# Optimization experiments

Hardware: AMD Instinct MI355X
Metric: run time of the kernel (lower is better)

Reference implementation:

```python
import jax, jax.numpy as jnp
import numpy as np

F = 6      # num_factors (== nodes per sample)
H = 32     # hidden_dim
B = 65536  # batch of samples (vectorized version of the per-sample Python loop)


def setup_inputs() -> dict:
    key = jax.random.key(0)
    ks = jax.random.split(key, 20)
    p = lambda k, shape: (jax.random.normal(k, shape, dtype=jnp.float32) * 0.1)
    inp = {
        "factors": jax.random.normal(ks[0], (B, F, F), dtype=jnp.float32),
        # CausalStructureLearner.node_encoder: Linear(F, H)
        "Wn": p(ks[1], (F, H)), "bn": p(ks[2], (H,)),
        # edge_predictor: Linear(2H, H) -> ReLU -> Linear(H, 1) -> Sigmoid
        "We1": p(ks[3], (2 * H, H)), "be1": p(ks[4], (H,)),
        "We2": p(ks[5], (H, 1)), "be2": p(ks[6], (1,)),
        # DynamicsPredictor.dynamics_net: F->H->H->F
        "Wd1": p(ks[7], (F, H)), "bd1": p(ks[8], (H,)),
        "Wd2": p(ks[9], (H, H)), "bd2": p(ks[10], (H,)),
        "Wd3": p(ks[11], (H, F)), "bd3": p(ks[12], (F,)),
        # AnomalyScorer.score_net: 3F->32->16->1 -> Sigmoid
        "Ws1": p(ks[13], (3 * F, 32)), "bs1": p(ks[14], (32,)),
        "Ws2": p(ks[15], (32, 16)), "bs2": p(ks[16], (16,)),
        "Ws3": p(ks[17], (16, 1)), "bs3": p(ks[18], (1,)),
    }
    return inp


def reference(factors, Wn, bn, We1, be1, We2, be2,
              Wd1, bd1, Wd2, bd2, Wd3, bd3,
              Ws1, bs1, Ws2, bs2, Ws3, bs3):
    # --- CausalStructureLearner (vectorized pairwise edge scoring) ---
    nf = factors @ Wn + bn                                  # [B, F, H]
    src = jnp.broadcast_to(nf[:, :, None, :], (B, F, F, H))  # node i
    dst = jnp.broadcast_to(nf[:, None, :, :], (B, F, F, H))  # node j
    pair = jnp.concatenate([src, dst], axis=-1)             # [B, F, F, 2H]
    eh = jax.nn.relu(pair @ We1 + be1)                       # [B, F, F, H]
    adj = jax.nn.sigmoid((eh @ We2 + be2)[..., 0])           # [B, F, F]
    adj = adj * (1.0 - jnp.eye(F, dtype=adj.dtype))          # zero diagonal

    # --- DynamicsPredictor: (adj @ factors.T).T == factors @ adj^T ---
    structured = jnp.einsum('bij,bnj->bni', adj, factors)    # [B, F(nodes), F]
    h = jax.nn.relu(structured @ Wd1 + bd1)
    h = jax.nn.relu(h @ Wd2 + bd2)
    pred = h @ Wd3 + bd3                                     # [B, F, F]

    # --- AnomalyScorer ---
    diff = jnp.abs(factors - pred)
    si = jnp.concatenate([factors, pred, diff], axis=-1)     # [B, F, 3F]
    s = jax.nn.relu(si @ Ws1 + bs1)
    s = jax.nn.relu(s @ Ws2 + bs2)
    s = jax.nn.sigmoid(s @ Ws3 + bs3)                        # [B, F, 1]
    scores = jnp.mean(s, axis=(1, 2))                        # [B]

    return adj, pred, scores
```

## Files before the change

kernel.cpp:

```cpp
#include <hip/hip_runtime.h>
#include <math.h>

typedef _Float16 half8 __attribute__((ext_vector_type(8)));

#define NT  256
#define SPB 84

#define FH_REC   0
#define FH_WD1   256
#define FH_WD2   352
#define FH_WD3T  864
#define FH_WS1   960
#define FH_WS2   1248
#define FH_WS3   1504
#define FF_BD1   1512
#define FF_BD2   1544
#define FF_BD3   1576
#define FF_BS1   1584
#define FF_BS2   1616
#define FF_MISC  1632
#define W_TOTF   1640

#define ADJ_STRIDE 52

__device__ __forceinline__ float sigmoidf_(float x) {
    return 1.0f / (1.0f + __expf(-x));
}

__global__ __launch_bounds__(512) void fold_kernel(
        const float* __restrict__ Wn,  const float* __restrict__ bn,
        const float* __restrict__ We1, const float* __restrict__ be1,
        const float* __restrict__ We2, const float* __restrict__ be2,
        const float* __restrict__ Wd1, const float* __restrict__ bd1,
        const float* __restrict__ Wd2, const float* __restrict__ bd2,
        const float* __restrict__ Wd3, const float* __restrict__ bd3,
        const float* __restrict__ Ws1, const float* __restrict__ bs1,
        const float* __restrict__ Ws2, const float* __restrict__ bs2,
        const float* __restrict__ Ws3, const float* __restrict__ bs3,
        float* __restrict__ cat) {
    _Float16* cath = (_Float16*)cat;
    const int t = threadIdx.x;
    {
        const int h = t >> 4, sl = t & 15;
        float val = 0.0f;
        if (sl < 6) {
            #pragma unroll
            for (int k = 0; k < 32; ++k) val = fmaf(Wn[sl*32+k], We1[k*32+h], val);
        } else if (sl < 12) {
            const int m = sl - 6;
            #pragma unroll
            for (int k = 0; k < 32; ++k) val = fmaf(Wn[m*32+k], We1[(32+k)*32+h], val);
        } else if (sl == 12) {
            #pragma unroll
            for (int k = 0; k < 32; ++k) val = fmaf(bn[k], We1[k*32+h] + We1[(32+k)*32+h], val);
            val += be1[h];
        } else if (sl == 13) {
            val = We2[h];
        }
        cath[h*16 + sl] = (_Float16)val;
    }
    for (int i = 512 + t; i < 3024; i += 512) {
        float v = 0.0f;
        if      (i < 704)  v = Wd1[i - 512];
        else if (i < 1728) v = Wd2[i - 704];
        else if (i < 1920) { const int q = i - 1728; v = Wd3[(q & 31)*6 + (q >> 5)]; }
        else if (i < 2496) v = Ws1[i - 1920];
        else if (i < 3008) v = Ws2[i - 2496];
        else               v = Ws3[i - 3008];
        cath[i] = (_Float16)v;
    }
    if (t < 128) {
        const int q = t;
        float v = 0.0f;
        if      (q < 32)  v = bd1[q];
        else if (q < 64)  v = bd2[q-32];
        else if (q < 70)  v = bd3[q-64];
        else if (q < 72)  v = 0.0f;
        else if (q < 104) v = bs1[q-72];
        else if (q < 120) v = bs2[q-104];
        else if (q == 120) v = bs3[0];
        else if (q == 121) v = be2[0];
        cat[1512 + q] = v;
    }
}

__global__ __launch_bounds__(NT, 1) void fused5_kernel(
        const float* __restrict__ factors, const float* __restrict__ cat,
        float* __restrict__ adj_out, float* __restrict__ pred_out,
        float* __restrict__ scores, int B) {
    __shared__ __align__(16) float Wsh[W_TOTF];
    __shared__ __align__(16) float adj_s[SPB * ADJ_STRIDE];
    __shared__ float sc_s[SPB * 6];

    const int t = threadIdx.x;
    #pragma unroll
    for (int i0 = 0; i0 < 2048; i0 += NT * 4) {
        const int i = i0 + t * 4;
        if (i < W_TOTF)
            *reinterpret_cast<float4*>(&Wsh[i]) = *reinterpret_cast<const float4*>(&cat[i]);
    }

    const int s = t / 3;
    const int n = t - s * 3;
    const int b = blockIdx.x * SPB + s;
    const bool act = (t < SPB * 3);
    const int sl_ = (s < SPB) ? s : (SPB - 1);
    const bool bv = act && (b < B);

    float fall[36], fi0[6], fi1[6];
    #pragma unroll
    for (int q = 0; q < 36; ++q) fall[q] = 0.0f;
    #pragma unroll
    for (int m = 0; m < 6; ++m) { fi0[m] = 0.0f; fi1[m] = 0.0f; }
    if (bv) {
        const float* f = factors + (size_t)b * 36;
        #pragma unroll
        for (int q = 0; q < 9; ++q) {
            const float4 v = reinterpret_cast<const float4*>(f)[q];
            fall[q*4+0] = v.x; fall[q*4+1] = v.y; fall[q*4+2] = v.z; fall[q*4+3] = v.w;
        }
        #pragma unroll
        for (int m = 0; m < 6; ++m) { fi0[m] = fall[n*6 + m]; fi1[m] = fall[(n+3)*6 + m]; }
    }
    __syncthreads();

    float av0[6], av1[6];
    {
        float acc0[6] = {0.f,0.f,0.f,0.f,0.f,0.f};
        float acc1[6] = {0.f,0.f,0.f,0.f,0.f,0.f};
        #pragma unroll 4
        for (int h = 0; h < 32; ++h) {
            const half8 ha = *reinterpret_cast<const half8*>(&Wsh[FH_REC + h*8]);
            const half8 hb = *reinterpret_cast<const half8*>(&Wsh[FH_REC + h*8 + 4]);
            const float A0=(float)ha[0], A1=(float)ha[1], A2=(float)ha[2];
            const float A3=(float)ha[3], A4=(float)ha[4], A5=(float)ha[5];
            const float B0=(float)ha[6], B1=(float)ha[7], B2=(float)hb[0];
            const float B3=(float)hb[1], B4=(float)hb[2], B5=(float)hb[3];
            const float c0=(float)hb[4], w2=(float)hb[5];
            float uh0 = c0, uh1 = c0;
            uh0 = fmaf(fi0[0], A0, uh0); uh1 = fmaf(fi1[0], A0, uh1);
            uh0 = fmaf(fi0[1], A1, uh0); uh1 = fmaf(fi1[1], A1, uh1);
            uh0 = fmaf(fi0[2], A2, uh0); uh1 = fmaf(fi1[2], A2, uh1);
            uh0 = fmaf(fi0[3], A3, uh0); uh1 = fmaf(fi1[3], A3, uh1);
            uh0 = fmaf(fi0[4], A4, uh0); uh1 = fmaf(fi1[4], A4, uh1);
            uh0 = fmaf(fi0[5], A5, uh0); uh1 = fmaf(fi1[5], A5, uh1);
            #pragma unroll
            for (int j = 0; j < 6; ++j) {
                float vj = fall[j*6+0] * B0;
                vj = fmaf(fall[j*6+1], B1, vj);
                vj = fmaf(fall[j*6+2], B2, vj);
                vj = fmaf(fall[j*6+3], B3, vj);
                vj = fmaf(fall[j*6+4], B4, vj);
                vj = fmaf(fall[j*6+5], B5, vj);
                acc0[j] = fmaf(fmaxf(uh0 + vj, 0.0f), w2, acc0[j]);
                acc1[j] = fmaf(fmaxf(uh1 + vj, 0.0f), w2, acc1[j]);
            }
        }
        const float b2 = Wsh[FF_MISC + 1];
        #pragma unroll
        for (int j = 0; j < 6; ++j) {
            av0[j] = (j == n)     ? 0.0f : sigmoidf_(acc0[j] + b2);
            av1[j] = (j == n + 3) ? 0.0f : sigmoidf_(acc1[j] + b2);
        }
    }
    if (act) {
        float* as = &adj_s[sl_ * ADJ_STRIDE];
        *reinterpret_cast<float4*>(&as[n*8])       = make_float4(av0[0], av0[1], av0[2], av0[3]);
        *reinterpret_cast<float2*>(&as[n*8+4])     = make_float2(av0[4], av0[5]);
        *reinterpret_cast<float4*>(&as[(n+3)*8])   = make_float4(av1[0], av1[1], av1[2], av1[3]);
        *reinterpret_cast<float2*>(&as[(n+3)*8+4]) = make_float2(av1[4], av1[5]);
    }
    if (bv) {
        float* ao = adj_out + (size_t)b * 36 + n * 6;
        *reinterpret_cast<float2*>(&ao[0])  = make_float2(av0[0], av0[1]);
        *reinterpret_cast<float2*>(&ao[2])  = make_float2(av0[2], av0[3]);
        *reinterpret_cast<float2*>(&ao[4])  = make_float2(av0[4], av0[5]);
        *reinterpret_cast<float2*>(&ao[18]) = make_float2(av1[0], av1[1]);
        *reinterpret_cast<float2*>(&ao[20]) = make_float2(av1[2], av1[3]);
        *reinterpret_cast<float2*>(&ao[22]) = make_float2(av1[4], av1[5]);
    }
    __syncthreads();

    float st0[6], st1[6];
    {
        const float* as = &adj_s[sl_ * ADJ_STRIDE];
        #pragma unroll
        for (int i = 0; i < 6; ++i) {
            const float4 qa = *reinterpret_cast<const float4*>(&as[i*8]);
            const float2 qb = *reinterpret_cast<const float2*>(&as[i*8+4]);
            float v = fi0[0] * qa.x;
            v = fmaf(fi0[1], qa.y, v); v = fmaf(fi0[2], qa.z, v);
            v = fmaf(fi0[3], qa.w, v); v = fmaf(fi0[4], qb.x, v);
            v = fmaf(fi0[5], qb.y, v);
            st0[i] = v;
            float w = fi1[0] * qa.x;
            w = fmaf(fi1[1], qa.y, w); w = fmaf(fi1[2], qa.z, w);
            w = fmaf(fi1[3], qa.w, w); w = fmaf(fi1[4], qb.x, w);
            w = fmaf(fi1[5], qb.y, w);
            st1[i] = w;
        }
    }

    float h1a[32], h1b[32];
    #pragma unroll
    for (int o4 = 0; o4 < 8; ++o4) {
        const float4 v = *reinterpret_cast<const float4*>(&Wsh[FF_BD1 + o4*4]);
        h1a[o4*4+0] = v.x; h1a[o4*4+1] = v.y; h1a[o4*4+2] = v.z; h1a[o4*4+3] = v.w;
        h1b[o4*4+0] = v.x; h1b[o4*4+1] = v.y; h1b[o4*4+2] = v.z; h1b[o4*4+3] = v.w;
    }
    #pragma unroll
    for (int m = 0; m < 6; ++m) {
        const float xa = st0[m], xb = st1[m];
        #pragma unroll
        for (int q = 0; q < 4; ++q) {
            const half8 w = *reinterpret_cast<const half8*>(&Wsh[FH_WD1 + m*16 + q*4]);
            #pragma unroll
            for (int e = 0; e < 8; ++e) {
                const float wf = (float)w[e];
                h1a[q*8+e] = fmaf(xa, wf, h1a[q*8+e]);
                h1b[q*8+e] = fmaf(xb, wf, h1b[q*8+e]);
            }
        }
    }
    #pragma unroll
    for (int o = 0; o < 32; ++o) { h1a[o] = fmaxf(h1a[o], 0.0f); h1b[o] = fmaxf(h1b[o], 0.0f); }

    float h2a[32], h2b[32];
    #pragma unroll
    for (int o4 = 0; o4 < 8; ++o4) {
        const float4 v = *reinterpret_cast<const float4*>(&Wsh[FF_BD2 + o4*4]);
        h2a[o4*4+0] = v.x; h2a[o4*4+1] = v.y; h2a[o4*4+2] = v.z; h2a[o4*4+3] = v.w;
        h2b[o4*4+0] = v.x; h2b[o4*4+1] = v.y; h2b[o4*4+2] = v.z; h2b[o4*4+3] = v.w;
    }
    #pragma unroll
    for (int p = 0; p < 2; ++p) {
        #pragma unroll
        for (int k = 0; k < 32; ++k) {
            const half8 w0 = *reinterpret_cast<const half8*>(&Wsh[FH_WD2 + k*16 + p*8]);
            const half8 w1 = *reinterpret_cast<const half8*>(&Wsh[FH_WD2 + k*16 + p*8 + 4]);
            const float xa = h1a[k], xb = h1b[k];
            #pragma unroll
            for (int e = 0; e < 8; ++e) {
                const float we0 = (float)w0[e], we1 = (float)w1[e];
                h2a[p*16+e]   = fmaf(xa, we0, h2a[p*16+e]);
                h2b[p*16+e]   = fmaf(xb, we0, h2b[p*16+e]);
                h2a[p*16+8+e] = fmaf(xa, we1, h2a[p*16+8+e]);
                h2b[p*16+8+e] = fmaf(xb, we1, h2b[p*16+8+e]);
            }
        }
    }
    #pragma unroll
    for (int o = 0; o < 32; ++o) { h2a[o] = fmaxf(h2a[o], 0.0f); h2b[o] = fmaxf(h2b[o], 0.0f); }

    float pra[6], prb[6];
    #pragma unroll
    for (int j = 0; j < 6; ++j) {
        float va = Wsh[FF_BD3 + j], vb = va;
        #pragma unroll
        for (int q = 0; q < 4; ++q) {
            const half8 w = *reinterpret_cast<const half8*>(&Wsh[FH_WD3T + j*16 + q*4]);
            #pragma unroll
            for (int e = 0; e < 8; ++e) {
                const float wf = (float)w[e];
                va = fmaf(h2a[q*8+e], wf, va);
                vb = fmaf(h2b[q*8+e], wf, vb);
            }
        }
        pra[j] = va; prb[j] = vb;
    }
    if (bv) {
        float* po = pred_out + (size_t)b * 36 + n * 6;
        *reinterpret_cast<float2*>(&po[0])  = make_float2(pra[0], pra[1]);
        *reinterpret_cast<float2*>(&po[2])  = make_float2(pra[2], pra[3]);
        *reinterpret_cast<float2*>(&po[4])  = make_float2(pra[4], pra[5]);
        *reinterpret_cast<float2*>(&po[18]) = make_float2(prb[0], prb[1]);
        *reinterpret_cast<float2*>(&po[20]) = make_float2(prb[2], prb[3]);
        *reinterpret_cast<float2*>(&po[22]) = make_float2(prb[4], prb[5]);
    }

    float dfa[6], dfb[6];
    #pragma unroll
    for (int j = 0; j < 6; ++j) { dfa[j] = fabsf(fi0[j] - pra[j]); dfb[j] = fabsf(fi1[j] - prb[j]); }

    float s1a[32], s1b[32];
    #pragma unroll
    for (int o4 = 0; o4 < 8; ++o4) {
        const float4 v = *reinterpret_cast<const float4*>(&Wsh[FF_BS1 + o4*4]);
        s1a[o4*4+0] = v.x; s1a[o4*4+1] = v.y; s1a[o4*4+2] = v.z; s1a[o4*4+3] = v.w;
        s1b[o4*4+0] = v.x; s1b[o4*4+1] = v.y; s1b[o4*4+2] = v.z; s1b[o4*4+3] = v.w;
    }
    #pragma unroll
    for (int m = 0; m < 6; ++m) {
        const float aa = fi0[m], pa = pra[m], da = dfa[m];
        const float ab = fi1[m], pb = prb[m], db = dfb[m];
        #pragma unroll
        for (int q = 0; q < 4; ++q) {
            const half8 wa = *reinterpret_cast<const half8*>(&Wsh[FH_WS1 + m*16 + q*4]);
            const half8 wp = *reinterpret_cast<const half8*>(&Wsh[FH_WS1 + (6+m)*16 + q*4]);
            const half8 wd = *reinterpret_cast<const half8*>(&Wsh[FH_WS1 + (12+m)*16 + q*4]);
            #pragma unroll
            for (int e = 0; e < 8; ++e) {
                const int o = q*8 + e;
                const float x1 = (float)wa[e], x2 = (float)wp[e], x3 = (float)wd[e];
                s1a[o] = fmaf(aa, x1, fmaf(pa, x2, fmaf(da, x3, s1a[o])));
                s1b[o] = fmaf(ab, x1, fmaf(pb, x2, fmaf(db, x3, s1b[o])));
            }
        }
    }
    #pragma unroll
    for (int o = 0; o < 32; ++o) { s1a[o] = fmaxf(s1a[o], 0.0f); s1b[o] = fmaxf(s1b[o], 0.0f); }

    float s2a[16], s2b[16];
    #pragma unroll
    for (int o4 = 0; o4 < 4; ++o4) {
        const float4 v = *reinterpret_cast<const float4*>(&Wsh[FF_BS2 + o4*4]);
        s2a[o4*4+0] = v.x; s2a[o4*4+1] = v.y; s2a[o4*4+2] = v.z; s2a[o4*4+3] = v.w;
        s2b[o4*4+0] = v.x; s2b[o4*4+1] = v.y; s2b[o4*4+2] = v.z; s2b[o4*4+3] = v.w;
    }
    #pragma unroll
    for (int k = 0; k < 32; ++k) {
        const half8 w0 = *reinterpret_cast<const half8*>(&Wsh[FH_WS2 + k*8]);
        const half8 w1 = *reinterpret_cast<const half8*>(&Wsh[FH_WS2 + k*8 + 4]);
        const float xa = s1a[k], xb = s1b[k];
        #pragma unroll
        for (int e = 0; e < 8; ++e) {
            const float we0 = (float)w0[e], we1 = (float)w1[e];
            s2a[e]   = fmaf(xa, we0, s2a[e]);
            s2b[e]   = fmaf(xb, we0, s2b[e]);
            s2a[8+e] = fmaf(xa, we1, s2a[8+e]);
            s2b[8+e] = fmaf(xb, we1, s2b[8+e]);
        }
    }
    #pragma unroll
    for (int o = 0; o < 16; ++o) { s2a[o] = fmaxf(s2a[o], 0.0f); s2b[o] = fmaxf(s2b[o], 0.0f); }

    {
        const half8 w0 = *reinterpret_cast<const half8*>(&Wsh[FH_WS3]);
        const half8 w1 = *reinterpret_cast<const half8*>(&Wsh[FH_WS3 + 4]);
        float s3a = Wsh[FF_MISC], s3b = s3a;
        #pragma unroll
        for (int e = 0; e < 8; ++e) {
            const float we0 = (float)w0[e], we1 = (float)w1[e];
            s3a = fmaf(s2a[e], we0, s3a);   s3b = fmaf(s2b[e], we0, s3b);
            s3a = fmaf(s2a[8+e], we1, s3a); s3b = fmaf(s2b[8+e], we1, s3b);
        }
        if (act) {
            sc_s[sl_*6 + n]     = sigmoidf_(s3a);
            sc_s[sl_*6 + n + 3] = sigmoidf_(s3b);
        }
    }
    __syncthreads();

    if (bv && n == 0) {
        const float sum = sc_s[sl_*6+0] + sc_s[sl_*6+1] + sc_s[sl_*6+2]
                        + sc_s[sl_*6+3] + sc_s[sl_*6+4] + sc_s[sl_*6+5];
        scores[b] = sum * (1.0f / 6.0f);
    }
}

extern "C" void kernel_launch(void* const* d_in, const int* in_sizes, int n_in,
                              void* d_out, int out_size, void* d_ws, size_t ws_size,
                              hipStream_t stream) {
    const float* factors = (const float*)d_in[0];
    const float* Wn  = (const float*)d_in[1];
    const float* bn  = (const float*)d_in[2];
    const float* We1 = (const float*)d_in[3];
    const float* be1 = (const float*)d_in[4];
    const float* We2 = (const float*)d_in[5];
    const float* be2 = (const float*)d_in[6];
    const float* Wd1 = (const float*)d_in[7];
    const float* bd1 = (const float*)d_in[8];
    const float* Wd2 = (const float*)d_in[9];
    const float* bd2 = (const float*)d_in[10];
    const float* Wd3 = (const float*)d_in[11];
    const float* bd3 = (const float*)d_in[12];
    const float* Ws1 = (const float*)d_in[13];
    const float* bs1 = (const float*)d_in[14];
    const float* Ws2 = (const float*)d_in[15];
    const float* bs2 = (const float*)d_in[16];
    const float* Ws3 = (const float*)d_in[17];
    const float* bs3 = (const float*)d_in[18];

    const int B = in_sizes[0] / 36;

    float* adj_out  = (float*)d_out;
    float* pred_out = (float*)d_out + (size_t)B * 36;
    float* scores   = (float*)d_out + (size_t)B * 72;
    float* cat      = (float*)d_ws;

    hipLaunchKernelGGL(fold_kernel, dim3(1), dim3(512), 0, stream,
                       Wn, bn, We1, be1, We2, be2,
                       Wd1, bd1, Wd2, bd2, Wd3, bd3,
                       Ws1, bs1, Ws2, bs2, Ws3, bs3, cat);

    const int nblocks = (B + SPB - 1) / SPB;
    hipLaunchKernelGGL(fused5_kernel, dim3(nblocks), dim3(NT), 0, stream,
                       factors, cat, adj_out, pred_out, scores, B);
}
```

Before: 174.2 us.

## Assign one node row per thread and spread weight folding across blocks

The main kernel now maps one node row per thread, with six threads per sample, instead of two rows per thread across three threads. This halves samples per block and launch bounds allow two blocks per CU, so per-thread register use drops and occupancy rises. The cost is that each thread recomputes the per-column edge terms (vj) over all six source rows, and shared-memory weight staging is repeated for twice as many blocks. The fold kernel is also split across eight blocks so its serial loops run in parallel.

```diff
diff --git a/kernel.cpp b/kernel.cpp
--- a/kernel.cpp
+++ b/kernel.cpp
@@ -4,7 +4,7 @@
 typedef _Float16 half8 __attribute__((ext_vector_type(8)));
 
 #define NT  256
-#define SPB 84
+#define SPB 42
 
 #define FH_REC   0
 #define FH_WD1   256
@@ -40,7 +40,8 @@
         float* __restrict__ cat) {
     _Float16* cath = (_Float16*)cat;
     const int t = threadIdx.x;
-    {
+    const int bid = blockIdx.x;
+    if (bid == 0) {
         const int h = t >> 4, sl = t & 15;
         float val = 0.0f;
         if (sl < 6) {
@@ -58,33 +59,36 @@
             val = We2[h];
         }
         cath[h*16 + sl] = (_Float16)val;
-    }
-    for (int i = 512 + t; i < 3024; i += 512) {
-        float v = 0.0f;
-        if      (i < 704)  v = Wd1[i - 512];
-        else if (i < 1728) v = Wd2[i - 704];
-        else if (i < 1920) { const int q = i - 1728; v = Wd3[(q & 31)*6 + (q >> 5)]; }
-        else if (i < 2496) v = Ws1[i - 1920];
-        else if (i < 3008) v = Ws2[i - 2496];
-        else               v = Ws3[i - 3008];
-        cath[i] = (_Float16)v;
-    }
-    if (t < 128) {
-        const int q = t;
-        float v = 0.0f;
-        if      (q < 32)  v = bd1[q];
-        else if (q < 64)  v = bd2[q-32];
-        else if (q < 70)  v = bd3[q-64];
-        else if (q < 72)  v = 0.0f;
-        else if (q < 104) v = bs1[q-72];
-        else if (q < 120) v = bs2[q-104];
-        else if (q == 120) v = bs3[0];
-        else if (q == 121) v = be2[0];
-        cat[1512 + q] = v;
+    } else if (bid <= 5) {
+        const int i = 512 + (bid - 1) * 512 + t;
+        if (i < 3024) {
+            float v = 0.0f;
+            if      (i < 704)  v = Wd1[i - 512];
+            else if (i < 1728) v = Wd2[i - 704];
+            else if (i < 1920) { const int q = i - 1728; v = Wd3[(q & 31)*6 + (q >> 5)]; }
+            else if (i < 2496) v = Ws1[i - 1920];
+            else if (i < 3008) v = Ws2[i - 2496];
+            else               v = Ws3[i - 3008];
+            cath[i] = (_Float16)v;
+        }
+    } else if (bid == 6) {
+        if (t < 128) {
+            const int q = t;
+            float v = 0.0f;
+            if      (q < 32)  v = bd1[q];
+            else if (q < 64)  v = bd2[q-32];
+            else if (q < 70)  v = bd3[q-64];
+            else if (q < 72)  v = 0.0f;
+            else if (q < 104) v = bs1[q-72];
+            else if (q < 120) v = bs2[q-104];
+            else if (q == 120) v = bs3[0];
+            else if (q == 121) v = be2[0];
+            cat[1512 + q] = v;
+        }
     }
 }
 
-__global__ __launch_bounds__(NT, 1) void fused5_kernel(
+__global__ __launch_bounds__(NT, 2) void fused7_kernel(
         const float* __restrict__ factors, const float* __restrict__ cat,
         float* __restrict__ adj_out, float* __restrict__ pred_out,
         float* __restrict__ scores, int B) {
@@ -100,18 +104,18 @@
             *reinterpret_cast<float4*>(&Wsh[i]) = *reinterpret_cast<const float4*>(&cat[i]);
     }
 
-    const int s = t / 3;
-    const int n = t - s * 3;
+    const int s = t / 6;
+    const int n = t - s * 6;
     const int b = blockIdx.x * SPB + s;
-    const bool act = (t < SPB * 3);
+    const bool act = (t < SPB * 6);
+    const bool bv = act && (b < B);
     const int sl_ = (s < SPB) ? s : (SPB - 1);
-    const bool bv = act && (b < B);
-
-    float fall[36], fi0[6], fi1[6];
+
+    float fall[36], fi[6];
     #pragma unroll
     for (int q = 0; q < 36; ++q) fall[q] = 0.0f;
     #pragma unroll
-    for (int m = 0; m < 6; ++m) { fi0[m] = 0.0f; fi1[m] = 0.0f; }
+    for (int m = 0; m < 6; ++m) fi[m] = 0.0f;
     if (bv) {
         const float* f = factors + (size_t)b * 36;
         #pragma unroll
@@ -119,118 +123,97 @@
             const float4 v = reinterpret_cast<const float4*>(f)[q];
             fall[q*4+0] = v.x; fall[q*4+1] = v.y; fall[q*4+2] = v.z; fall[q*4+3] = v.w;
         }
-        #pragma unroll
-        for (int m = 0; m < 6; ++m) { fi0[m] = fall[n*6 + m]; fi1[m] = fall[(n+3)*6 + m]; }
+        const float* fr = f + n * 6;
+        #pragma unroll
+        for (int q = 0; q < 3; ++q) {
+            const float2 v = reinterpret_cast<const float2*>(fr)[q];
+            fi[q*2+0] = v.x; fi[q*2+1] = v.y;
+        }
     }
     __syncthreads();
 
-    float av0[6], av1[6];
+    float av[6];
     {
-        float acc0[6] = {0.f,0.f,0.f,0.f,0.f,0.f};
-        float acc1[6] = {0.f,0.f,0.f,0.f,0.f,0.f};
+        float acc[6] = {0.f,0.f,0.f,0.f,0.f,0.f};
         #pragma unroll 4
         for (int h = 0; h < 32; ++h) {
             const half8 ha = *reinterpret_cast<const half8*>(&Wsh[FH_REC + h*8]);
             const half8 hb = *reinterpret_cast<const half8*>(&Wsh[FH_REC + h*8 + 4]);
-            const float A0=(float)ha[0], A1=(float)ha[1], A2=(float)ha[2];
-            const float A3=(float)ha[3], A4=(float)ha[4], A5=(float)ha[5];
-            const float B0=(float)ha[6], B1=(float)ha[7], B2=(float)hb[0];
-            const float B3=(float)hb[1], B4=(float)hb[2], B5=(float)hb[3];
-            const float c0=(float)hb[4], w2=(float)hb[5];
-            float uh0 = c0, uh1 = c0;
-            uh0 = fmaf(fi0[0], A0, uh0); uh1 = fmaf(fi1[0], A0, uh1);
-            uh0 = fmaf(fi0[1], A1, uh0); uh1 = fmaf(fi1[1], A1, uh1);
-            uh0 = fmaf(fi0[2], A2, uh0); uh1 = fmaf(fi1[2], A2, uh1);
-            uh0 = fmaf(fi0[3], A3, uh0); uh1 = fmaf(fi1[3], A3, uh1);
-            uh0 = fmaf(fi0[4], A4, uh0); uh1 = fmaf(fi1[4], A4, uh1);
-            uh0 = fmaf(fi0[5], A5, uh0); uh1 = fmaf(fi1[5], A5, uh1);
+            float uh = (float)hb[4];
+            uh = fmaf(fi[0], (float)ha[0], uh);
+            uh = fmaf(fi[1], (float)ha[1], uh);
+            uh = fmaf(fi[2], (float)ha[2], uh);
+            uh = fmaf(fi[3], (float)ha[3], uh);
+            uh = fmaf(fi[4], (float)ha[4], uh);
+            uh = fmaf(fi[5], (float)ha[5], uh);
+            const float w2 = (float)hb[5];
             #pragma unroll
             for (int j = 0; j < 6; ++j) {
-                float vj = fall[j*6+0] * B0;
-                vj = fmaf(fall[j*6+1], B1, vj);
-                vj = fmaf(fall[j*6+2], B2, vj);
-                vj = fmaf(fall[j*6+3], B3, vj);
-                vj = fmaf(fall[j*6+4], B4, vj);
-                vj = fmaf(fall[j*6+5], B5, vj);
-                acc0[j] = fmaf(fmaxf(uh0 + vj, 0.0f), w2, acc0[j]);
-                acc1[j] = fmaf(fmaxf(uh1 + vj, 0.0f), w2, acc1[j]);
+                float vj =      fall[j*6+0] * (float)ha[6];
+                vj = fmaf(fall[j*6+1], (float)ha[7], vj);
+                vj = fmaf(fall[j*6+2], (float)hb[0], vj);
+                vj = fmaf(fall[j*6+3], (float)hb[1], vj);
+                vj = fmaf(fall[j*6+4], (float)hb[2], vj);
+                vj = fmaf(fall[j*6+5], (float)hb[3], vj);
+                acc[j] = fmaf(fmaxf(uh + vj, 0.0f), w2, acc[j]);
             }
         }
         const float b2 = Wsh[FF_MISC + 1];
         #pragma unroll
-        for (int j = 0; j < 6; ++j) {
-            av0[j] = (j == n)     ? 0.0f : sigmoidf_(acc0[j] + b2);
-            av1[j] = (j == n + 3) ? 0.0f : sigmoidf_(acc1[j] + b2);
-        }
+        for (int j = 0; j < 6; ++j) av[j] = (j == n) ? 0.0f : sigmoidf_(acc[j] + b2);
     }
     if (act) {
-        float* as = &adj_s[sl_ * ADJ_STRIDE];
-        *reinterpret_cast<float4*>(&as[n*8])       = make_float4(av0[0], av0[1], av0[2], av0[3]);
-        *reinterpret_cast<float2*>(&as[n*8+4])     = make_float2(av0[4], av0[5]);
-        *reinterpret_cast<float4*>(&as[(n+3)*8])   = make_float4(av1[0], av1[1], av1[2], av1[3]);
-        *reinterpret_cast<float2*>(&as[(n+3)*8+4]) = make_float2(av1[4], av1[5]);
+        float* as = &adj_s[sl_ * ADJ_STRIDE + n * 8];
+        *reinterpret_cast<float4*>(&as[0]) = make_float4(av[0], av[1], av[2], av[3]);
+        *reinterpret_cast<float2*>(&as[4]) = make_float2(av[4], av[5]);
     }
     if (bv) {
         float* ao = adj_out + (size_t)b * 36 + n * 6;
-        *reinterpret_cast<float2*>(&ao[0])  = make_float2(av0[0], av0[1]);
-        *reinterpret_cast<float2*>(&ao[2])  = make_float2(av0[2], av0[3]);
-        *reinterpret_cast<float2*>(&ao[4])  = make_float2(av0[4], av0[5]);
-        *reinterpret_cast<float2*>(&ao[18]) = make_float2(av1[0], av1[1]);
-        *reinterpret_cast<float2*>(&ao[20]) = make_float2(av1[2], av1[3]);
-        *reinterpret_cast<float2*>(&ao[22]) = make_float2(av1[4], av1[5]);
+        *reinterpret_cast<float2*>(&ao[0]) = make_float2(av[0], av[1]);
+        *reinterpret_cast<float2*>(&ao[2]) = make_float2(av[2], av[3]);
+        *reinterpret_cast<float2*>(&ao[4]) = make_float2(av[4], av[5]);
     }
     __syncthreads();
 
-    float st0[6], st1[6];
+    float st[6];
     {
         const float* as = &adj_s[sl_ * ADJ_STRIDE];
         #pragma unroll
         for (int i = 0; i < 6; ++i) {
             const float4 qa = *reinterpret_cast<const float4*>(&as[i*8]);
             const float2 qb = *reinterpret_cast<const float2*>(&as[i*8+4]);
-            float v = fi0[0] * qa.x;
-            v = fmaf(fi0[1], qa.y, v); v = fmaf(fi0[2], qa.z, v);
-            v = fmaf(fi0[3], qa.w, v); v = fmaf(fi0[4], qb.x, v);
-            v = fmaf(fi0[5], qb.y, v);
-            st0[i] = v;
-            float w = fi1[0] * qa.x;
-            w = fmaf(fi1[1], qa.y, w); w = fmaf(fi1[2], qa.z, w);
-            w = fmaf(fi1[3], qa.w, w); w = fmaf(fi1[4], qb.x, w);
-            w = fmaf(fi1[5], qb.y, w);
-            st1[i] = w;
-        }
-    }
-
-    float h1a[32], h1b[32];
+            float v = fi[0] * qa.x;
+            v = fmaf(fi[1], qa.y, v); v = fmaf(fi[2], qa.z, v);
+            v = fmaf(fi[3], qa.w, v); v = fmaf(fi[4], qb.x, v);
+            v = fmaf(fi[5], qb.y, v);
+            st[i] = v;
+        }
+    }
+
+    float h1[32];
     #pragma unroll
     for (int o4 = 0; o4 < 8; ++o4) {
         const float4 v = *reinterpret_cast<const float4*>(&Wsh[FF_BD1 + o4*4]);
-        h1a[o4*4+0] = v.x; h1a[o4*4+1] = v.y; h1a[o4*4+2] = v.z; h1a[o4*4+3] = v.w;
-        h1b[o4*4+0] = v.x; h1b[o4*4+1] = v.y; h1b[o4*4+2] = v.z; h1b[o4*4+3] = v.w;
+        h1[o4*4+0] = v.x; h1[o4*4+1] = v.y; h1[o4*4+2] = v.z; h1[o4*4+3] = v.w;
     }
     #pragma unroll
     for (int m = 0; m < 6; ++m) {
-        const float xa = st0[m], xb = st1[m];
+        const float x = st[m];
         #pragma unroll
         for (int q = 0; q < 4; ++q) {
             const half8 w = *reinterpret_cast<const half8*>(&Wsh[FH_WD1 + m*16 + q*4]);
             #pragma unroll
-            for (int e = 0; e < 8; ++e) {
-                const float wf = (float)w[e];
-                h1a[q*8+e] = fmaf(xa, wf, h1a[q*8+e]);
-                h1b[q*8+e] = fmaf(xb, wf, h1b[q*8+e]);
-            }
-        }
-    }
-    #pragma unroll
-    for (int o = 0; o < 32; ++o) { h1a[o] = fmaxf(h1a[o], 0.0f); h1b[o] = fmaxf(h1b[o], 0.0f); }
-
-    float h2a[32], h2b[32];
+            for (int e = 0; e < 8; ++e) h1[q*8+e] = fmaf(x, (float)w[e], h1[q*8+e]);
+        }
+    }
+    #pragma unroll
+    for (int o = 0; o < 32; ++o) h1[o] = fmaxf(h1[o], 0.0f);
+
+    float h2[32];
     #pragma unroll
     for (int o4 = 0; o4 < 8; ++o4) {
         const float4 v = *reinterpret_cast<const float4*>(&Wsh[FF_BD2 + o4*4]);
-        h2a[o4*4+0] = v.x; h2a[o4*4+1] = v.y; h2a[o4*4+2] = v.z; h2a[o4*4+3] = v.w;
-        h2b[o4*4+0] = v.x; h2b[o4*4+1] = v.y; h2b[o4*4+2] = v.z; h2b[o4*4+3] = v.w;
+        h2[o4*4+0] = v.x; h2[o4*4+1] = v.y; h2[o4*4+2] = v.z; h2[o4*4+3] = v.w;
     }
     #pragma unroll
     for (int p = 0; p < 2; ++p) {
@@ -238,61 +221,49 @@
         for (int k = 0; k < 32; ++k) {
             const half8 w0 = *reinterpret_cast<const half8*>(&Wsh[FH_WD2 + k*16 + p*8]);
             const half8 w1 = *reinterpret_cast<const half8*>(&Wsh[FH_WD2 + k*16 + p*8 + 4]);
-            const float xa = h1a[k], xb = h1b[k];
+            const float x = h1[k];
             #pragma unroll
             for (int e = 0; e < 8; ++e) {
-                const float we0 = (float)w0[e], we1 = (float)w1[e];
-                h2a[p*16+e]   = fmaf(xa, we0, h2a[p*16+e]);
-                h2b[p*16+e]   = fmaf(xb, we0, h2b[p*16+e]);
-                h2a[p*16+8+e] = fmaf(xa, we1, h2a[p*16+8+e]);
-                h2b[p*16+8+e] = fmaf(xb, we1, h2b[p*16+8+e]);
+                h2[p*16+e]   = fmaf(x, (float)w0[e], h2[p*16+e]);
+                h2[p*16+8+e] = fmaf(x, (float)w1[e], h2[p*16+8+e]);
             }
         }
     }
     #pragma unroll
-    for (int o = 0; o < 32; ++o) { h2a[o] = fmaxf(h2a[o], 0.0f); h2b[o] = fmaxf(h2b[o], 0.0f); }
-
-    float pra[6], prb[6];
+    for (int o = 0; o < 32; ++o) h2[o] = fmaxf(h2[o], 0.0f);
+
+    float pr[6];
     #pragma unroll
     for (int j = 0; j < 6; ++j) {
-        float va = Wsh[FF_BD3 + j], vb = va;
+        float v = Wsh[FF_BD3 + j];
         #pragma unroll
         for (int q = 0; q < 4; ++q) {
             const half8 w = *reinterpret_cast<const half8*>(&Wsh[FH_WD3T + j*16 + q*4]);
             #pragma unroll
-            for (int e = 0; e < 8; ++e) {
-                const float wf = (float)w[e];
-                va = fmaf(h2a[q*8+e], wf, va);
-                vb = fmaf(h2b[q*8+e], wf, vb);
-            }
-        }
-        pra[j] = va; prb[j] = vb;
+            for (int e = 0; e < 8; ++e) v = fmaf(h2[q*8+e], (float)w[e], v);
+        }
+        pr[j] = v;
     }
     if (bv) {
         float* po = pred_out + (size_t)b * 36 + n * 6;
-        *reinterpret_cast<float2*>(&po[0])  = make_float2(pra[0], pra[1]);
-        *reinterpret_cast<float2*>(&po[2])  = make_float2(pra[2], pra[3]);
-        *reinterpret_cast<float2*>(&po[4])  = make_float2(pra[4], pra[5]);
-        *reinterpret_cast<float2*>(&po[18]) = make_float2(prb[0], prb[1]);
-        *reinterpret_cast<float2*>(&po[20]) = make_float2(prb[2], prb[3]);
-        *reinterpret_cast<float2*>(&po[22]) = make_float2(prb[4], prb[5]);
-    }
-
-    float dfa[6], dfb[6];
-    #pragma unroll
-    for (int j = 0; j < 6; ++j) { dfa[j] = fabsf(fi0[j] - pra[j]); dfb[j] = fabsf(fi1[j] - prb[j]); }
-
-    float s1a[32], s1b[32];
+        *reinterpret_cast<float2*>(&po[0]) = make_float2(pr[0], pr[1]);
+        *reinterpret_cast<float2*>(&po[2]) = make_float2(pr[2], pr[3]);
+        *reinterpret_cast<float2*>(&po[4]) = make_float2(pr[4], pr[5]);
+    }
+
+    float df[6];
+    #pragma unroll
+    for (int j = 0; j < 6; ++j) df[j] = fabsf(fi[j] - pr[j]);
+
+    float s1[32];
     #pragma unroll
     for (int o4 = 0; o4 < 8; ++o4) {
         const float4 v = *reinterpret_cast<const float4*>(&Wsh[FF_BS1 + o4*4]);
-        s1a[o4*4+0] = v.x; s1a[o4*4+1] = v.y; s1a[o4*4+2] = v.z; s1a[o4*4+3] = v.w;
-        s1b[o4*4+0] = v.x; s1b[o4*4+1] = v.y; s1b[o4*4+2] = v.z; s1b[o4*4+3] = v.w;
+        s1[o4*4+0] = v.x; s1[o4*4+1] = v.y; s1[o4*4+2] = v.z; s1[o4*4+3] = v.w;
     }
     #pragma unroll
     for (int m = 0; m < 6; ++m) {
-        const float aa = fi0[m], pa = pra[m], da = dfa[m];
-        const float ab = fi1[m], pb = prb[m], db = dfb[m];
+        const float a = fi[m], p = pr[m], d = df[m];
         #pragma unroll
         for (int q = 0; q < 4; ++q) {
             const half8 wa = *reinterpret_cast<const half8*>(&Wsh[FH_WS1 + m*16 + q*4]);
@@ -301,53 +272,43 @@
             #pragma unroll
             for (int e = 0; e < 8; ++e) {
                 const int o = q*8 + e;
-                const float x1 = (float)wa[e], x2 = (float)wp[e], x3 = (float)wd[e];
-                s1a[o] = fmaf(aa, x1, fmaf(pa, x2, fmaf(da, x3, s1a[o])));
-                s1b[o] = fmaf(ab, x1, fmaf(pb, x2, fmaf(db, x3, s1b[o])));
+                s1[o] = fmaf(a, (float)wa[e], fmaf(p, (float)wp[e], fmaf(d, (float)wd[e], s1[o])));
             }
         }
     }
     #pragma unroll
-    for (int o = 0; o < 32; ++o) { s1a[o] = fmaxf(s1a[o], 0.0f); s1b[o] = fmaxf(s1b[o], 0.0f); }
-
-    float s2a[16], s2b[16];
+    for (int o = 0; o < 32; ++o) s1[o] = fmaxf(s1[o], 0.0f);
+
+    float s2[16];
     #pragma unroll
     for (int o4 = 0; o4 < 4; ++o4) {
         const float4 v = *reinterpret_cast<const float4*>(&Wsh[FF_BS2 + o4*4]);
-        s2a[o4*4+0] = v.x; s2a[o4*4+1] = v.y; s2a[o4*4+2] = v.z; s2a[o4*4+3] = v.w;
-        s2b[o4*4+0] = v.x; s2b[o4*4+1] = v.y; s2b[o4*4+2] = v.z; s2b[o4*4+3] = v.w;
+        s2[o4*4+0] = v.x; s2[o4*4+1] = v.y; s2[o4*4+2] = v.z; s2[o4*4+3] = v.w;
     }
     #pragma unroll
     for (int k = 0; k < 32; ++k) {
         const half8 w0 = *reinterpret_cast<const half8*>(&Wsh[FH_WS2 + k*8]);
         const half8 w1 = *reinterpret_cast<const half8*>(&Wsh[FH_WS2 + k*8 + 4]);
-        const float xa = s1a[k], xb = s1b[k];
+        const float x = s1[k];
         #pragma unroll
         for (int e = 0; e < 8; ++e) {
-            const float we0 = (float)w0[e], we1 = (float)w1[e];
-            s2a[e]   = fmaf(xa, we0, s2a[e]);
-            s2b[e]   = fmaf(xb, we0, s2b[e]);
-            s2a[8+e] = fmaf(xa, we1, s2a[8+e]);
-            s2b[8+e] = fmaf(xb, we1, s2b[8+e]);
-        }
-    }
-    #pragma unroll
-    for (int o = 0; o < 16; ++o) { s2a[o] = fmaxf(s2a[o], 0.0f); s2b[o] = fmaxf(s2b[o], 0.0f); }
+            s2[e]   = fmaf(x, (float)w0[e], s2[e]);
+            s2[8+e] = fmaf(x, (float)w1[e], s2[8+e]);
+        }
+    }
+    #pragma unroll
+    for (int o = 0; o < 16; ++o) s2[o] = fmaxf(s2[o], 0.0f);
 
     {
         const half8 w0 = *reinterpret_cast<const half8*>(&Wsh[FH_WS3]);
         const half8 w1 = *reinterpret_cast<const half8*>(&Wsh[FH_WS3 + 4]);
-        float s3a = Wsh[FF_MISC], s3b = s3a;
+        float s3 = Wsh[FF_MISC];
         #pragma unroll
         for (int e = 0; e < 8; ++e) {
-            const float we0 = (float)w0[e], we1 = (float)w1[e];
-            s3a = fmaf(s2a[e], we0, s3a);   s3b = fmaf(s2b[e], we0, s3b);
-            s3a = fmaf(s2a[8+e], we1, s3a); s3b = fmaf(s2b[8+e], we1, s3b);
-        }
-        if (act) {
-            sc_s[sl_*6 + n]     = sigmoidf_(s3a);
-            sc_s[sl_*6 + n + 3] = sigmoidf_(s3b);
-        }
+            s3 = fmaf(s2[e],   (float)w0[e], s3);
+            s3 = fmaf(s2[8+e], (float)w1[e], s3);
+        }
+        if (act) sc_s[sl_ * 6 + n] = sigmoidf_(s3);
     }
     __syncthreads();
 
@@ -388,12 +349,12 @@
     float* scores   = (float*)d_out + (size_t)B * 72;
     float* cat      = (float*)d_ws;
 
-    hipLaunchKernelGGL(fold_kernel, dim3(1), dim3(512), 0, stream,
+    hipLaunchKernelGGL(fold_kernel, dim3(8), dim3(512), 0, stream,
                        Wn, bn, We1, be1, We2, be2,
                        Wd1, bd1, Wd2, bd2, Wd3, bd3,
                        Ws1, bs1, Ws2, bs2, Ws3, bs3, cat);
 
     const int nblocks = (B + SPB - 1) / SPB;
-    hipLaunchKernelGGL(fused5_kernel, dim3(nblocks), dim3(NT), 0, stream,
+    hipLaunchKernelGGL(fused7_kernel, dim3(nblocks), dim3(NT), 0, stream,
                        factors, cat, adj_out, pred_out, scores, B);
 }
```

New measurement: 163.7 us. -6.0%, faster.
